# Optimization experiments

Hardware: AMD Instinct MI355X
Metric: run time of the kernel (lower is better)

The kernel has to match this reference:

```python
import jax, jax.numpy as jnp
from jax import lax
import numpy as np

B, N, D = 64, 1025, 384   # tokens = 1 CLS + 32x32 patch grid
G = 32
K = 8                      # num rotation bases
KS = 8                     # num scale bases
R = 8                      # rank of skew bases
H = 128                    # controller hidden dim
CIN = 3 * D                # cls_mean_var pooling
OUT = D
ROT_GATE_BIAS = -4.0
LOCAL_GATE_BIAS = -3.0


def setup_inputs() -> dict:
    key = jax.random.key(0)
    ks = jax.random.split(key, 16)
    f32 = jnp.float32
    inp = {
        "x": jax.random.normal(ks[0], (B, N, D), f32),
        "shared_weight": jax.random.normal(ks[1], (OUT, D), f32) * 0.02,
        "bias": jnp.zeros((OUT,), f32),
        "left_basis": jax.random.normal(ks[2], (K, D, R), f32) * 0.02,
        "right_basis": jax.random.normal(ks[3], (K, D, R), f32) * 0.02,
        "scale_basis": jax.random.normal(ks[4], (KS, OUT), f32) * 0.01,
        "scale_strength": jnp.asarray(0.25, f32),
        "dw_kernel": jax.random.normal(ks[5], (D, 1, 3, 3), f32) * 0.1,  # depthwise 3x3
        "ctrl_w1": jax.random.normal(ks[6], (H, CIN), f32) * 0.02,
        "ctrl_b1": jnp.zeros((H,), f32),
        "w_rot": jax.random.normal(ks[7], (K, H), f32) * 0.02,
        "b_rot": jnp.zeros((K,), f32),
        "w_rgate": jax.random.normal(ks[8], (1, H), f32) * 0.02,
        "b_rgate": jnp.full((1,), ROT_GATE_BIAS, f32),
        "w_lgate": jax.random.normal(ks[9], (1, H), f32) * 0.02,
        "b_lgate": jnp.full((1,), LOCAL_GATE_BIAS, f32),
        "w_scale": jax.random.normal(ks[10], (KS, H), f32) * 0.02,
        "b_scale": jnp.zeros((KS,), f32),
    }
    return inp


def _forward(x, shared_weight, bias, left_basis, right_basis, scale_basis,
             scale_strength, dw_kernel, ctrl_w1, ctrl_b1, w_rot, b_rot,
             w_rgate, b_rgate, w_lgate, b_lgate, w_scale, b_scale):
    b, n, d = x.shape
    # --- conditioning signal: cls | mean | var (unbiased=False) ---
    cls = x[:, 0]
    mean = jnp.mean(x, axis=1)
    var = jnp.var(x, axis=1)
    z = jnp.concatenate([cls, mean, var], axis=-1)          # [B, 3D]
    # --- controller MLP ---
    h = jax.nn.gelu(z @ ctrl_w1.T + ctrl_b1)                 # [B, H]
    rot_coeff = jnp.tanh(h @ w_rot.T + b_rot)                # [B, K]
    rot_gate = jax.nn.sigmoid(h @ w_rgate.T + b_rgate)[:, 0] # [B]
    local_gate = jax.nn.sigmoid(h @ w_lgate.T + b_lgate)[:, 0]
    scale_coeff = jnp.tanh(h @ w_scale.T + b_scale)          # [B, KS]
    # --- gated local depthwise-conv mixer on the patch grid ---
    cls_tok = x[:, :1, :]
    patch = x[:, 1:, :]                                      # [B, G*G, D]
    grid = patch.transpose(0, 2, 1).reshape(b, d, G, G)      # NCHW
    local = lax.conv_general_dilated(
        grid, dw_kernel, window_strides=(1, 1), padding="SAME",
        feature_group_count=d, dimension_numbers=("NCHW", "OIHW", "NCHW"))
    local_tok = local.reshape(b, d, G * G).transpose(0, 2, 1)
    mixed_patch = patch + local_gate[:, None, None] * (local_tok - patch)
    lm = jnp.concatenate([cls_tok, mixed_patch], axis=1)     # [B, N, D]
    # --- normalized skew bases from low-rank factors ---
    basis = (jnp.einsum("kdr,ker->kde", left_basis, right_basis)
             - jnp.einsum("kdr,ker->kde", right_basis, left_basis))  # [K, D, D]
    norm = jnp.maximum(jnp.linalg.norm(basis.reshape(K, -1), axis=1), 1e-6)
    basis = basis / norm[:, None, None]
    # --- per-sample Cayley rotation (fp32 solve) ---
    skew = jnp.einsum("bk,kde->bde", rot_coeff, basis)       # residual_scale = 1.0
    eye = jnp.eye(d, dtype=jnp.float32)
    half = 0.5 * skew
    transform = jnp.linalg.solve(eye - half, jnp.broadcast_to(eye, half.shape) + half)
    transform = transform.astype(x.dtype)
    # --- gated rotation of features ---
    rotated = jnp.einsum("bnd,bdh->bnh", lm, transform)
    mixed = lm + rot_gate[:, None, None] * (rotated - lm)
    # --- shared linear + dynamic output scaling ---
    preact = mixed @ shared_weight.T + bias                  # [B, N, OUT]
    scale_delta = jnp.tanh(scale_coeff @ scale_basis)        # [B, OUT]
    scale = 1.0 + scale_strength * scale_delta[:, None, :]
    return preact * scale


def reference(x, shared_weight, bias, left_basis, right_basis, scale_basis,
              scale_strength, dw_kernel, ctrl_w1, ctrl_b1, w_rot, b_rot,
              w_rgate, b_rgate, w_lgate, b_lgate, w_scale, b_scale):
    return _forward(x, shared_weight, bias, left_basis, right_basis, scale_basis,
                    scale_strength, dw_kernel, ctrl_w1, ctrl_b1, w_rot, b_rot,
                    w_rgate, b_rgate, w_lgate, b_lgate, w_scale, b_scale)
```

## Files before the change

kernel.cpp:

```cpp
#include <hip/hip_runtime.h>
#include <hip/hip_bf16.h>
#include <math.h>

static const int Bb = 64, Nn = 1025, Dd = 384, Kk = 8, Rr = 8, Hh = 128, CINc = 1152, OUTo = 384;

#define OFF_PSTAT 0u
#define OFF_RC    475136u
#define OFF_RG    475648u
#define OFF_LG    475712u
#define OFF_SCALE 476288u
#define OFF_N2    505472u
#define OFF_P     505600u
#define OFF_Q     554752u
#define OFF_G     603904u
#define OFF_QW    620288u
#define OFF_PB    669440u
#define OFF_EP    694016u
#define OFF_ZT    3839744u
#define OFF_WBT   5412608u
#define OFF_LM    10131200u

typedef __attribute__((ext_vector_type(8))) short short8;
typedef __attribute__((ext_vector_type(8))) __bf16 bf16x8;
typedef __attribute__((ext_vector_type(4))) float f32x4;

#define MFMA_BF16(a,b,c) __builtin_amdgcn_mfma_f32_16x16x32_bf16( \
    __builtin_bit_cast(bf16x8,(a)), __builtin_bit_cast(bf16x8,(b)), (c), 0, 0, 0)

#define GLDS16(gp, lp) __builtin_amdgcn_global_load_lds( \
    (__attribute__((address_space(1))) void*)(gp), \
    (__attribute__((address_space(3))) void*)(lp), 16, 0, 0)

__device__ __forceinline__ float gelu_t(float v){
    float u = 0.7978845608028654f*(v + 0.044715f*v*v*v);
    return 0.5f*v*(1.0f + tanhf(u));
}
__device__ __forceinline__ float sigm(float v){ return 1.0f/(1.0f+expf(-v)); }
__device__ __forceinline__ unsigned short f2bf(float v){
    return __builtin_bit_cast(unsigned short, __float2bfloat16(v));
}

__global__ __launch_bounds__(384) void k_stats(const float* __restrict__ x, float* __restrict__ ps){
    int s = blockIdx.x, b = blockIdx.y, t = threadIdx.x;
    int dq = t % 96, ng = t / 96;
    int n0 = s*129, n1 = n0+129 < Nn ? n0+129 : Nn;
    const float4* xb = (const float4*)(x + (size_t)b*Nn*Dd);
    float4 sm = make_float4(0.f,0.f,0.f,0.f), sq = make_float4(0.f,0.f,0.f,0.f);
    for (int n = n0+ng; n < n1; n += 4){
        float4 v = xb[(size_t)n*96 + dq];
        sm.x += v.x; sm.y += v.y; sm.z += v.z; sm.w += v.w;
        sq.x += v.x*v.x; sq.y += v.y*v.y; sq.z += v.z*v.z; sq.w += v.w*v.w;
    }
    __shared__ float4 smS[384];
    __shared__ float4 sqS[384];
    smS[t] = sm; sqS[t] = sq;
    __syncthreads();
    if (t < 96){
        float4 a0 = smS[t], a1 = smS[t+96], a2 = smS[t+192], a3 = smS[t+288];
        float4 q0 = sqS[t], q1 = sqS[t+96], q2 = sqS[t+192], q3 = sqS[t+288];
        float4 a = make_float4(a0.x+a1.x+a2.x+a3.x, a0.y+a1.y+a2.y+a3.y, a0.z+a1.z+a2.z+a3.z, a0.w+a1.w+a2.w+a3.w);
        float4 q = make_float4(q0.x+q1.x+q2.x+q3.x, q0.y+q1.y+q2.y+q3.y, q0.z+q1.z+q2.z+q3.z, q0.w+q1.w+q2.w+q3.w);
        ((float4*)(ps + ((size_t)(b*8+s)*2+0)*Dd))[t] = a;
        ((float4*)(ps + ((size_t)(b*8+s)*2+1)*Dd))[t] = q;
    }
}

__global__ __launch_bounds__(384) void k_ctrl(const float* __restrict__ x, const float* __restrict__ ps,
    const float* __restrict__ w1, const float* __restrict__ b1,
    const float* __restrict__ w_rot, const float* __restrict__ b_rot,
    const float* __restrict__ w_rg, const float* __restrict__ b_rg,
    const float* __restrict__ w_lg, const float* __restrict__ b_lg,
    const float* __restrict__ w_sc, const float* __restrict__ b_sc,
    const float* __restrict__ sbasis, const float* __restrict__ sstr,
    float* __restrict__ rc, float* __restrict__ rg, float* __restrict__ lg,
    float* __restrict__ scalev, unsigned short* __restrict__ lm){
    __shared__ float zs[1152];
    __shared__ float hp[3*128];
    __shared__ float hs[128];
    __shared__ float scl[8];
    int b = blockIdx.x, t = threadIdx.x;
    float sm = 0.f, sq = 0.f;
    for (int s = 0; s < 8; ++s){
        sm += ps[((size_t)(b*8+s)*2+0)*Dd + t];
        sq += ps[((size_t)(b*8+s)*2+1)*Dd + t];
    }
    float mean = sm*(1.0f/Nn);
    float var  = sq*(1.0f/Nn) - mean*mean;
    float cls  = x[(size_t)b*Nn*Dd + t];
    zs[t] = cls; zs[Dd + t] = mean; zs[2*Dd + t] = var;
    lm[(size_t)b*Nn*Dd + t] = f2bf(cls);
    __syncthreads();
    {
        int row = t & 127, part = t >> 7;
        const float* wrow = w1 + (size_t)row*CINc + part*384;
        const float* zp = zs + part*384;
        float acc = 0.f;
        for (int c = 0; c < 384; ++c) acc += zp[c]*wrow[c];
        hp[part*128 + row] = acc;
    }
    __syncthreads();
    if (t < 128)
        hs[t] = gelu_t(hp[t] + hp[128+t] + hp[256+t] + b1[t]);
    __syncthreads();
    if (t < 8){
        float acc = b_rot[t]; const float* w = w_rot + (size_t)t*Hh;
        for (int c = 0; c < Hh; ++c) acc += hs[c]*w[c];
        rc[b*8+t] = tanhf(acc);
    } else if (t == 8){
        float acc = b_rg[0];
        for (int c = 0; c < Hh; ++c) acc += hs[c]*w_rg[c];
        rg[b] = sigm(acc);
    } else if (t == 9){
        float acc = b_lg[0];
        for (int c = 0; c < Hh; ++c) acc += hs[c]*w_lg[c];
        lg[b] = sigm(acc);
    } else if (t < 18){
        int q = t-10; float acc = b_sc[q]; const float* w = w_sc + (size_t)q*Hh;
        for (int c = 0; c < Hh; ++c) acc += hs[c]*w[c];
        scl[q] = tanhf(acc);
    }
    __syncthreads();
    float acc = 0.f;
    #pragma unroll
    for (int q = 0; q < 8; ++q) acc += scl[q]*sbasis[q*OUTo + t];
    scalev[(size_t)b*OUTo + t] = 1.0f + sstr[0]*tanhf(acc);
}

__global__ __launch_bounds__(256) void k_prep(const float* __restrict__ lb, const float* __restrict__ rb,
                                              float* __restrict__ n2, float* __restrict__ P,
                                              float* __restrict__ Q, unsigned short* __restrict__ Pb){
    int bid = blockIdx.x, t = threadIdx.x;
    if (bid < 8){
        if (t < 64){
            int k = bid;
            int r = t >> 3, s = t & 7;
            const float* L = lb + (size_t)k*Dd*Rr;
            const float* R = rb + (size_t)k*Dd*Rr;
            float a = 0.f, bsum = 0.f, c = 0.f, c2 = 0.f;
            for (int d = 0; d < Dd; ++d){
                float lr = L[d*8+r], ls = L[d*8+s], rr = R[d*8+r], rs = R[d*8+s];
                a += lr*ls; bsum += rr*rs; c += lr*rs; c2 += ls*rr;
            }
            float contrib = a*bsum - c*c2;
            for (int m = 32; m > 0; m >>= 1) contrib += __shfl_xor(contrib, m, 64);
            if (t == 0) n2[k] = 2.f*contrib;
        }
    } else {
        int idx = (bid-8)*256 + t;
        int d = idx >> 7, j = idx & 127;
        int k = (j & 63) >> 3, r = j & 7;
        float lv = lb[((size_t)k*Dd + d)*Rr + r];
        float rv = rb[((size_t)k*Dd + d)*Rr + r];
        float pv = (j < 64) ? lv : rv;
        P[idx] = pv;
        Pb[idx] = f2bf(pv);
        Q[idx] = (j < 64) ? rv : lv;
    }
}

__global__ __launch_bounds__(512) void k_gramqw(const float* __restrict__ P, const float* __restrict__ Q,
                                                const float* __restrict__ Wsh,
                                                float* __restrict__ G, float* __restrict__ QW){
    __shared__ float qc[384];
    int i = blockIdx.x, t = threadIdx.x;
    for (int d = t; d < Dd; d += 512) qc[d] = Q[d*128 + i];
    __syncthreads();
    if (t < 128){
        float a = 0.f;
        for (int d = 0; d < Dd; ++d) a += qc[d]*P[d*128 + t];
        G[i*128 + t] = a;
    } else {
        int o = t - 128;
        float a = 0.f;
        const float* wrow = Wsh + (size_t)o*Dd;
        for (int d = 0; d < Dd; ++d) a += qc[d]*wrow[d];
        QW[(size_t)i*OUTo + o] = a;
    }
}

__global__ __launch_bounds__(512) void k_cayley(const float* __restrict__ G, const float* __restrict__ rc,
                                                const float* __restrict__ n2, const float* __restrict__ rg,
                                                float* __restrict__ Ep){
    __shared__ float GT[128*128];
    __shared__ float Xs[128*128];
    int b = blockIdx.x, t = threadIdx.x;
    for (int lin = t; lin < 16384; lin += 512){
        int i = lin >> 7, m = lin & 127;
        GT[m*128 + i] = G[lin];
    }
    int j0 = (t & 15)*8, i0 = (t >> 4)*4;
    float dj[8], di[4];
    #pragma unroll
    for (int u = 0; u < 8; ++u){
        int j = j0+u; int k = (j&63)>>3;
        float nrm = fmaxf(sqrtf(n2[k]), 1e-6f);
        float al = 0.5f*rc[b*8+k]/nrm;
        dj[u] = (j < 64) ? al : -al;
    }
    #pragma unroll
    for (int u = 0; u < 4; ++u){
        int i = i0+u; int k = (i&63)>>3;
        float nrm = fmaxf(sqrtf(n2[k]), 1e-6f);
        float al = 0.5f*rc[b*8+k]/nrm;
        di[u] = (i < 64) ? al : -al;
    }
    __syncthreads();
    float B0[4][8], acc[4][8];
    #pragma unroll
    for (int ui = 0; ui < 4; ++ui)
        #pragma unroll
        for (int uj = 0; uj < 8; ++uj){
            int i = i0+ui, j = j0+uj;
            float g = GT[j*128 + i];
            B0[ui][uj] = di[ui]*g*dj[uj] + ((i==j) ? di[ui] : 0.f);
        }
    #pragma unroll
    for (int ui = 0; ui < 4; ++ui)
        #pragma unroll
        for (int uj = 0; uj < 8; ++uj)
            Xs[(i0+ui)*128 + j0+uj] = B0[ui][uj];
    __syncthreads();
    for (int pass = 0; pass < 2; ++pass){
        #pragma unroll
        for (int ui = 0; ui < 4; ++ui)
            #pragma unroll
            for (int uj = 0; uj < 8; ++uj) acc[ui][uj] = 0.f;
        for (int m = 0; m < 128; ++m){
            float4 g4 = *(const float4*)&GT[m*128 + i0];
            float4 xa = *(const float4*)&Xs[m*128 + j0];
            float4 xb = *(const float4*)&Xs[m*128 + j0 + 4];
            float gi[4] = {g4.x, g4.y, g4.z, g4.w};
            float xv[8] = {xa.x, xa.y, xa.z, xa.w, xb.x, xb.y, xb.z, xb.w};
            #pragma unroll
            for (int ui = 0; ui < 4; ++ui)
                #pragma unroll
                for (int uj = 0; uj < 8; ++uj)
                    acc[ui][uj] += gi[ui]*xv[uj];
        }
        if (pass == 0){
            __syncthreads();
            #pragma unroll
            for (int ui = 0; ui < 4; ++ui)
                #pragma unroll
                for (int uj = 0; uj < 8; ++uj)
                    Xs[(i0+ui)*128 + j0+uj] = B0[ui][uj] + di[ui]*acc[ui][uj];
            __syncthreads();
        }
    }
    float rgb = rg[b];
    #pragma unroll
    for (int ui = 0; ui < 4; ++ui){
        int i = i0+ui;
        float o[8];
        #pragma unroll
        for (int uj = 0; uj < 8; ++uj){
            int j = j0+uj;
            float x2 = B0[ui][uj] + di[ui]*acc[ui][uj];
            o[uj] = rgb*(x2 + ((i==j) ? di[ui] : 0.f));
        }
        float4* ep4 = (float4*)(Ep + ((size_t)b*128 + i)*128 + j0);
        ep4[0] = make_float4(o[0], o[1], o[2], o[3]);
        ep4[1] = make_float4(o[4], o[5], o[6], o[7]);
    }
}

__global__ __launch_bounds__(384) void k_zmatT(const float* __restrict__ Ep, const float* __restrict__ QW, unsigned short* __restrict__ ZT){
    __shared__ float Es[4*128];
    int ig = blockIdx.x, b = blockIdx.y, t = threadIdx.x;
    int i0 = ig*4;
    for (int lin = t; lin < 512; lin += 384)
        Es[lin] = Ep[((size_t)b*128 + i0 + (lin >> 7))*128 + (lin & 127)];
    __syncthreads();
    float a0=0.f, a1=0.f, a2=0.f, a3=0.f;
    for (int m = 0; m < 128; ++m){
        float qw = QW[(size_t)m*OUTo + t];
        a0 += Es[m]*qw; a1 += Es[128+m]*qw; a2 += Es[256+m]*qw; a3 += Es[384+m]*qw;
    }
    ushort4 uv;
    uv.x = f2bf(a0); uv.y = f2bf(a1); uv.z = f2bf(a2); uv.w = f2bf(a3);
    *(ushort4*)(ZT + ((size_t)b*OUTo + t)*128 + i0) = uv;
}

__global__ __launch_bounds__(256) void k_wbt(const unsigned short* __restrict__ ZT, const unsigned short* __restrict__ Pb,
                                             const float* __restrict__ Wsh, unsigned short* __restrict__ WbT){
    __shared__ short8 As[256];
    __shared__ short8 Bs[256];
    int b = blockIdx.y;
    int mt = blockIdx.x/6, nt2 = blockIdx.x%6;
    int m0 = mt*64, n0 = nt2*64;
    int t = threadIdx.x;
    int w = t>>6, l = t&63;
    int wr = w>>1, wc = w&1;
    const unsigned short* Ab = ZT + (size_t)b*OUTo*128;
    int lrow = t>>2, lseg = t&3;
    f32x4 acc[2][2];
    #pragma unroll
    for (int mi=0;mi<2;++mi)
        #pragma unroll
        for (int ni=0;ni<2;++ni)
            #pragma unroll
            for (int q=0;q<4;++q) acc[mi][ni][q] = 0.f;
    for (int kt = 0; kt < 4; ++kt){
        int k0 = kt*32;
        short8 av = *(const short8*)(Ab + (size_t)(m0+lrow)*128 + k0 + lseg*8);
        short8 bv = *(const short8*)(Pb + (size_t)(n0+lrow)*128 + k0 + lseg*8);
        __syncthreads();
        As[lseg*64 + lrow] = av;
        Bs[lseg*64 + lrow] = bv;
        __syncthreads();
        short8 a0 = As[(l>>4)*64 + wr*32 + (l&15)];
        short8 a1 = As[(l>>4)*64 + wr*32 + 16 + (l&15)];
        short8 b0 = Bs[(l>>4)*64 + wc*32 + (l&15)];
        short8 b1 = Bs[(l>>4)*64 + wc*32 + 16 + (l&15)];
        acc[0][0] = MFMA_BF16(a0, b0, acc[0][0]);
        acc[0][1] = MFMA_BF16(a0, b1, acc[0][1]);
        acc[1][0] = MFMA_BF16(a1, b0, acc[1][0]);
        acc[1][1] = MFMA_BF16(a1, b1, acc[1][1]);
    }
    unsigned short* Wo = WbT + (size_t)b*OUTo*Dd;
    #pragma unroll
    for (int mi=0;mi<2;++mi){
        #pragma unroll
        for (int ni=0;ni<2;++ni){
            int col = n0 + wc*32 + ni*16 + (l&15);
            #pragma unroll
            for (int r=0;r<4;++r){
                int row = m0 + wr*32 + mi*16 + (l>>4)*4 + r;
                float v = Wsh[(size_t)row*Dd + col] + acc[mi][ni][r];
                Wo[(size_t)row*Dd + col] = f2bf(v);
            }
        }
    }
}

__global__ __launch_bounds__(384) void k_lm(const float* __restrict__ x, const float* __restrict__ kw,
                                            const float* __restrict__ lg, unsigned short* __restrict__ lm){
    __shared__ float kws[9*384];
    int flat = blockIdx.x;
    int work = (flat & 7)*256 + (flat >> 3);
    int b = work >> 5, gy = work & 31;
    int t = threadIdx.x;
    for (int i = t; i < 3456; i += 384){
        int d = i % 384, tap = i / 384;
        kws[tap*384 + d] = kw[d*9 + tap];
    }
    __syncthreads();
    int dq = t % 96, gxg = t / 96;
    float lgb = lg[b];
    const float4* xb = (const float4*)(x + (size_t)b*Nn*Dd);
    unsigned short* lmb = lm + (size_t)b*Nn*Dd;
    #pragma unroll
    for (int u = 0; u < 8; ++u){
        int gx = gxg + 4*u;
        int n = 1 + (gy << 5) + gx;
        float4 xc = xb[(size_t)n*96 + dq];
        float ax = 0.f, ay = 0.f, az = 0.f, aw = 0.f;
        #pragma unroll
        for (int ky = 0; ky < 3; ++ky){
            int yy = gy + ky - 1;
            if ((unsigned)yy < 32u){
                #pragma unroll
                for (int kx = 0; kx < 3; ++kx){
                    int xx = gx + kx - 1;
                    if ((unsigned)xx < 32u){
                        float4 xv = xb[(size_t)(1 + (yy << 5) + xx)*96 + dq];
                        const float4 kv = *(const float4*)(&kws[(ky*3+kx)*384 + dq*4]);
                        ax += xv.x*kv.x; ay += xv.y*kv.y; az += xv.z*kv.z; aw += xv.w*kv.w;
                    }
                }
            }
        }
        ushort4 o4;
        o4.x = f2bf(xc.x + lgb*(ax - xc.x));
        o4.y = f2bf(xc.y + lgb*(ay - xc.y));
        o4.z = f2bf(xc.z + lgb*(az - xc.z));
        o4.w = f2bf(xc.w + lgb*(aw - xc.w));
        *(ushort4*)(lmb + (size_t)n*Dd + dq*4) = o4;
    }
}

__global__ __launch_bounds__(256) void k_gemm_nt(const unsigned short* __restrict__ lm, const unsigned short* __restrict__ WbT,
                                                 const float* __restrict__ bias, const float* __restrict__ scalev,
                                                 float* __restrict__ out){
    __shared__ unsigned short smem[16384];
    __shared__ float svs[64];
    __shared__ float bvs[64];
    int flat = blockIdx.x;
    int work = (flat & 7)*816 + (flat >> 3);
    int b = work / 102;
    int r = work - b*102;
    int nt = r / 6, ot = r - nt*6;
    int n0 = nt*64, o0 = ot*64;
    int t = threadIdx.x;
    int w = t >> 6, l = t & 63;
    int wr = w >> 1, wc = w & 1;
    const unsigned short* Ab = lm + (size_t)b*Nn*Dd;
    const unsigned short* Bt = WbT + (size_t)b*OUTo*Dd;
    if (t < 64){ svs[t] = scalev[(size_t)b*OUTo + o0 + t]; bvs[t] = bias[o0 + t]; }
    int srow = l >> 3;
    int sch  = (l & 7) ^ srow;
    f32x4 acc[2][2];
    #pragma unroll
    for (int fi = 0; fi < 2; ++fi)
        #pragma unroll
        for (int fj = 0; fj < 2; ++fj)
            #pragma unroll
            for (int q = 0; q < 4; ++q) acc[fi][fj][q] = 0.f;

#define STAGE(bufi, k0) { \
    unsigned short* Adst = &smem[(bufi)*8192]; \
    unsigned short* Bdst = &smem[(bufi)*8192 + 4096]; \
    _Pragma("unroll") \
    for (int i = 0; i < 2; ++i){ \
        int r0 = (i*4 + w)*8; \
        GLDS16(Ab + (size_t)(n0 + r0 + srow)*Dd + (k0) + sch*8, Adst + r0*64); \
        GLDS16(Bt + (size_t)(o0 + r0 + srow)*Dd + (k0) + sch*8, Bdst + r0*64); \
    } }

    STAGE(0, 0);
    __syncthreads();
    int cur = 0;
    for (int kt = 0; kt < 6; ++kt){
        if (kt < 5) STAGE(cur^1, (kt+1)*64);
        const unsigned short* As  = &smem[cur*8192];
        const unsigned short* Bs2 = &smem[cur*8192 + 4096];
        #pragma unroll
        for (int kc = 0; kc < 2; ++kc){
            short8 a[2], bb[2];
            int ch = (kc*4 + (l>>4)) ^ (l&7);
            #pragma unroll
            for (int f = 0; f < 2; ++f){
                int ra  = wr*32 + f*16 + (l&15);
                int rb2 = wc*32 + f*16 + (l&15);
                a[f]  = *(const short8*)&As [ra*64  + ch*8];
                bb[f] = *(const short8*)&Bs2[rb2*64 + ch*8];
            }
            acc[0][0] = MFMA_BF16(a[0], bb[0], acc[0][0]);
            acc[0][1] = MFMA_BF16(a[0], bb[1], acc[0][1]);
            acc[1][0] = MFMA_BF16(a[1], bb[0], acc[1][0]);
            acc[1][1] = MFMA_BF16(a[1], bb[1], acc[1][1]);
        }
        __syncthreads();
        cur ^= 1;
    }
#undef STAGE
    float* Cs = (float*)smem;
    #pragma unroll
    for (int fi = 0; fi < 2; ++fi)
        #pragma unroll
        for (int fj = 0; fj < 2; ++fj){
            int col = wc*32 + fj*16 + (l&15);
            #pragma unroll
            for (int q = 0; q < 4; ++q){
                int row = wr*32 + fi*16 + (l>>4)*4 + q;
                Cs[row*68 + col] = acc[fi][fj][q];
            }
        }
    __syncthreads();
    #pragma unroll
    for (int p = 0; p < 4; ++p){
        int idx = p*256 + t;
        int row = idx >> 4, c4 = idx & 15;
        int gr = n0 + row;
        if (gr < Nn){
            float4 v = *(const float4*)&Cs[row*68 + c4*4];
            float4 o4;
            o4.x = svs[c4*4+0]*(bvs[c4*4+0] + v.x);
            o4.y = svs[c4*4+1]*(bvs[c4*4+1] + v.y);
            o4.z = svs[c4*4+2]*(bvs[c4*4+2] + v.z);
            o4.w = svs[c4*4+3]*(bvs[c4*4+3] + v.w);
            *(float4*)(out + ((size_t)b*Nn + gr)*OUTo + o0 + c4*4) = o4;
        }
    }
}

extern "C" void kernel_launch(void* const* d_in, const int* in_sizes, int n_in,
                              void* d_out, int out_size, void* d_ws, size_t ws_size,
                              hipStream_t stream){
    const float* x     = (const float*)d_in[0];
    const float* Wsh   = (const float*)d_in[1];
    const float* bias  = (const float*)d_in[2];
    const float* lb    = (const float*)d_in[3];
    const float* rb    = (const float*)d_in[4];
    const float* sbasis= (const float*)d_in[5];
    const float* sstr  = (const float*)d_in[6];
    const float* kw    = (const float*)d_in[7];
    const float* w1    = (const float*)d_in[8];
    const float* b1    = (const float*)d_in[9];
    const float* w_rot = (const float*)d_in[10];
    const float* b_rot = (const float*)d_in[11];
    const float* w_rg  = (const float*)d_in[12];
    const float* b_rg  = (const float*)d_in[13];
    const float* w_lg  = (const float*)d_in[14];
    const float* b_lg  = (const float*)d_in[15];
    const float* w_sc  = (const float*)d_in[16];
    const float* b_sc  = (const float*)d_in[17];
    float* out = (float*)d_out;
    float* ws  = (float*)d_ws;

    float* ps     = ws + OFF_PSTAT;
    float* rc     = ws + OFF_RC;
    float* rg     = ws + OFF_RG;
    float* lg     = ws + OFF_LG;
    float* scalev = ws + OFF_SCALE;
    float* n2     = ws + OFF_N2;
    float* P      = ws + OFF_P;
    float* Q      = ws + OFF_Q;
    float* G      = ws + OFF_G;
    float* QW     = ws + OFF_QW;
    unsigned short* Pb  = (unsigned short*)(ws + OFF_PB);
    float* Ep     = ws + OFF_EP;
    unsigned short* ZT  = (unsigned short*)(ws + OFF_ZT);
    unsigned short* WbT = (unsigned short*)(ws + OFF_WBT);
    unsigned short* lmb = (unsigned short*)(ws + OFF_LM);

    k_stats   <<<dim3(8, Bb), 384, 0, stream>>>(x, ps);
    k_ctrl    <<<Bb, 384, 0, stream>>>(x, ps, w1, b1, w_rot, b_rot, w_rg, b_rg, w_lg, b_lg,
                                       w_sc, b_sc, sbasis, sstr, rc, rg, lg, scalev, lmb);
    k_prep    <<<200, 256, 0, stream>>>(lb, rb, n2, P, Q, Pb);
    k_gramqw  <<<128, 512, 0, stream>>>(P, Q, Wsh, G, QW);
    k_cayley  <<<Bb, 512, 0, stream>>>(G, rc, n2, rg, Ep);
    k_zmatT   <<<dim3(32, Bb), 384, 0, stream>>>(Ep, QW, ZT);
    k_wbt     <<<dim3(36, Bb), 256, 0, stream>>>(ZT, Pb, Wsh, WbT);
    k_lm      <<<2048, 384, 0, stream>>>(x, kw, lg, lmb);
    k_gemm_nt <<<6528, 256, 0, stream>>>(lmb, WbT, bias, scalev, out);
}
```

Measured before the change: 254.6 us.

## Use three-stage K=32 LDS pipeline with explicit vmcnt waits in batched GEMM

Restructures the main batched GEMM's K loop from a double-buffered K=64 tile into a triple-buffered K=32 tile. Loads are issued two stages ahead, and explicit s_waitcnt vmcnt and raw s_barrier calls replace __syncthreads, so global-to-LDS loads overlap with MFMA work. The swizzle pattern changes to fit 32-wide rows, and LDS use drops, which may allow more resident blocks. The cost is more loop iterations and barriers per tile, plus fragile hand-counted vmcnt values.

```diff
diff --git a/kernel.cpp b/kernel.cpp
--- a/kernel.cpp
+++ b/kernel.cpp
@@ -382,7 +382,7 @@
 __global__ __launch_bounds__(256) void k_gemm_nt(const unsigned short* __restrict__ lm, const unsigned short* __restrict__ WbT,
                                                  const float* __restrict__ bias, const float* __restrict__ scalev,
                                                  float* __restrict__ out){
-    __shared__ unsigned short smem[16384];
+    __shared__ unsigned short smem[12288];
     __shared__ float svs[64];
     __shared__ float bvs[64];
     int flat = blockIdx.x;
@@ -397,8 +397,8 @@
     const unsigned short* Ab = lm + (size_t)b*Nn*Dd;
     const unsigned short* Bt = WbT + (size_t)b*OUTo*Dd;
     if (t < 64){ svs[t] = scalev[(size_t)b*OUTo + o0 + t]; bvs[t] = bias[o0 + t]; }
-    int srow = l >> 3;
-    int sch  = (l & 7) ^ srow;
+    int srow = l >> 2;
+    int gch  = (l & 3) ^ ((l >> 3) & 3);
     f32x4 acc[2][2];
     #pragma unroll
     for (int fi = 0; fi < 2; ++fi)
@@ -407,43 +407,38 @@
             #pragma unroll
             for (int q = 0; q < 4; ++q) acc[fi][fj][q] = 0.f;
 
-#define STAGE(bufi, k0) { \
-    unsigned short* Adst = &smem[(bufi)*8192]; \
-    unsigned short* Bdst = &smem[(bufi)*8192 + 4096]; \
-    _Pragma("unroll") \
-    for (int i = 0; i < 2; ++i){ \
-        int r0 = (i*4 + w)*8; \
-        GLDS16(Ab + (size_t)(n0 + r0 + srow)*Dd + (k0) + sch*8, Adst + r0*64); \
-        GLDS16(Bt + (size_t)(o0 + r0 + srow)*Dd + (k0) + sch*8, Bdst + r0*64); \
-    } }
-
-    STAGE(0, 0);
-    __syncthreads();
-    int cur = 0;
-    for (int kt = 0; kt < 6; ++kt){
-        if (kt < 5) STAGE(cur^1, (kt+1)*64);
-        const unsigned short* As  = &smem[cur*8192];
-        const unsigned short* Bs2 = &smem[cur*8192 + 4096];
-        #pragma unroll
-        for (int kc = 0; kc < 2; ++kc){
-            short8 a[2], bb[2];
-            int ch = (kc*4 + (l>>4)) ^ (l&7);
-            #pragma unroll
-            for (int f = 0; f < 2; ++f){
-                int ra  = wr*32 + f*16 + (l&15);
-                int rb2 = wc*32 + f*16 + (l&15);
-                a[f]  = *(const short8*)&As [ra*64  + ch*8];
-                bb[f] = *(const short8*)&Bs2[rb2*64 + ch*8];
-            }
-            acc[0][0] = MFMA_BF16(a[0], bb[0], acc[0][0]);
-            acc[0][1] = MFMA_BF16(a[0], bb[1], acc[0][1]);
-            acc[1][0] = MFMA_BF16(a[1], bb[0], acc[1][0]);
-            acc[1][1] = MFMA_BF16(a[1], bb[1], acc[1][1]);
-        }
-        __syncthreads();
-        cur ^= 1;
-    }
-#undef STAGE
+#define STG(bufi, k0) { \
+    unsigned short* Adst = &smem[(bufi)*4096 + (w*16)*32]; \
+    unsigned short* Bdst = &smem[(bufi)*4096 + 2048 + (w*16)*32]; \
+    GLDS16(Ab + (size_t)(n0 + w*16 + srow)*Dd + (k0) + gch*8, Adst); \
+    GLDS16(Bt + (size_t)(o0 + w*16 + srow)*Dd + (k0) + gch*8, Bdst); }
+
+    STG(0, 0);
+    STG(1, 32);
+    int rch = ((l>>4) ^ (((l&15)>>1)&3)) * 8;
+    int ra0 = (wr*32 + (l&15))*32;
+    int rb0 = (wc*32 + (l&15))*32;
+    for (int kt = 0; kt < 12; ++kt){
+        if (kt < 10) STG((kt+2)%3, (kt+2)*32);
+        if (kt < 10)       asm volatile("s_waitcnt vmcnt(4)" ::: "memory");
+        else if (kt == 10) asm volatile("s_waitcnt vmcnt(2)" ::: "memory");
+        else               asm volatile("s_waitcnt vmcnt(0)" ::: "memory");
+        __builtin_amdgcn_s_barrier();
+        __builtin_amdgcn_sched_barrier(0);
+        const unsigned short* As  = &smem[(kt%3)*4096];
+        const unsigned short* Bs2 = &smem[(kt%3)*4096 + 2048];
+        short8 a0 = *(const short8*)&As [ra0 + rch];
+        short8 a1 = *(const short8*)&As [ra0 + 512 + rch];
+        short8 b0 = *(const short8*)&Bs2[rb0 + rch];
+        short8 b1 = *(const short8*)&Bs2[rb0 + 512 + rch];
+        acc[0][0] = MFMA_BF16(a0, b0, acc[0][0]);
+        acc[0][1] = MFMA_BF16(a0, b1, acc[0][1]);
+        acc[1][0] = MFMA_BF16(a1, b0, acc[1][0]);
+        acc[1][1] = MFMA_BF16(a1, b1, acc[1][1]);
+        __builtin_amdgcn_sched_barrier(0);
+        __builtin_amdgcn_s_barrier();
+    }
+#undef STG
     float* Cs = (float*)smem;
     #pragma unroll
     for (int fi = 0; fi < 2; ++fi)
```

After: 261.9 us. 1.03x slower.
